# Performance work log

Hardware: AMD Instinct MI355X
Metric: run time of the kernel (lower is better)

## Reference

```python
import jax, jax.numpy as jnp
import numpy as np

B, T, N, FIN, FOUT, EDGE_DIM = 8, 16, 256, 32, 32, 16


def setup_inputs() -> dict:
    key = jax.random.key(0)
    ks = jax.random.split(key, 8)
    def xavier(k, shape):
        fan_in, fan_out = shape[0], shape[1]
        limit = float(np.sqrt(6.0 / (fan_in + fan_out)))
        return jax.random.uniform(k, shape, jnp.float32, -limit, limit)
    return {
        "x": jax.random.normal(ks[0], (B, T, N, FIN), jnp.float32),
        "adj": jax.random.uniform(ks[1], (N, N), jnp.float32),
        # edge_net: Linear(1, edge_dim) -> GELU -> Linear(edge_dim, Fin*Fout)
        "w1": xavier(ks[2], (1, EDGE_DIM)),
        "b1": jnp.zeros((EDGE_DIM,), jnp.float32),
        "w2": xavier(ks[3], (EDGE_DIM, FIN * FOUT)),
        "b2": jnp.zeros((FIN * FOUT,), jnp.float32),
        # node_lin: Linear(Fin, Fout)
        "node_w": xavier(ks[4], (FIN, FOUT)),
        "node_b": jnp.zeros((FOUT,), jnp.float32),
    }


def reference(x, adj, w1, b1, w2, b2, node_w, node_b):
    # edge-conditioned weights: (N, N, Fin, Fout)
    h = jax.nn.gelu(adj[:, :, None] * w1[0] + b1, approximate=False)  # (N,N,E)
    edge_w = (h @ w2 + b2).reshape(N, N, FIN, FOUT)
    # msg[b,t,i,j,:] = sum_f x[b,t,j,f] * edge_w[i,j,f,:]; agg = sum_j msg
    agg = jnp.einsum("btjf,ijfo->btio", x, edge_w)  # (B,T,N,Fout)
    y = jax.nn.gelu(x @ node_w + node_b + agg, approximate=False)
    return y
```

## Files before the change

### kernel.cpp

```cpp
#include <hip/hip_runtime.h>
#include <math.h>

#define NB    256
#define EDIM  16
#define FINN  32
#define FOUTN 32
#define BT    128
#define KKD   4096

typedef __attribute__((ext_vector_type(8))) short short8;
typedef __attribute__((ext_vector_type(4))) float floatx4;

#define MFMA16(a,b,c) __builtin_amdgcn_mfma_f32_16x16x32_bf16((a),(b),(c),0,0,0)

__device__ __forceinline__ float gelu_f(float v) {
    return 0.5f * v * (1.0f + erff(v * 0.70710678118654752f));
}
__device__ __forceinline__ ushort f2bf(float x) {
    union { float f; unsigned u; } v; v.f = x;
    unsigned r = (v.u + 0x7FFFu + ((v.u >> 16) & 1u)) >> 16;
    return (ushort)r;
}
__device__ __forceinline__ float bf2f(ushort b) {
    union { unsigned u; float f; } v; v.u = ((unsigned)b) << 16; return v.f;
}

__global__ __launch_bounds__(256) void h_kernel(const float* __restrict__ adj,
                                                const float* __restrict__ w1,
                                                const float* __restrict__ b1,
                                                const float* __restrict__ w2,
                                                ushort* __restrict__ Hf,
                                                ushort* __restrict__ w2f) {
    int tid = threadIdx.x;
    if (blockIdx.x >= 128) {
        for (int s = 0; s < 2048; s += 256) {
            int slot = s + tid;
            int e = slot >> 7, r = slot & 127;
            int ot = r >> 6, lane = r & 63;
            int m = lane & 15, quad = lane >> 4;
            const float* src = w2 + (size_t)e * 1024 + (quad * 8) * 32 + ot * 16 + m;
            ushort tmp[8];
            #pragma unroll
            for (int i = 0; i < 8; ++i) tmp[i] = f2bf(src[i * 32]);
            *(int4*)(w2f + (size_t)slot * 8) = *(int4*)tmp;
        }
        return;
    }
    __shared__ float adjs[16][264];
    __shared__ float w1s[16], b1s[16];
    int it = blockIdx.x & 15;
    int kq = blockIdx.x >> 4;
    if (tid < 16) { w1s[tid] = w1[tid]; b1s[tid] = b1[tid]; }
    #pragma unroll
    for (int q = 0; q < 4; ++q) {
        int u = q * 256 + tid;
        int row = u >> 6, c4 = u & 63;
        *(float4*)&adjs[row][c4 * 4] =
            ((const float4*)(adj + ((size_t)it * 16 + row) * 256))[c4];
    }
    __syncthreads();
    #pragma unroll
    for (int q = 0; q < 4; ++q) {
        int u = q * 256 + tid;
        int ks = kq * 16 + (u >> 6);
        int lane = u & 63;
        int m = lane & 15, quad = lane >> 4;
        int e = ks >> 3;
        int j0 = (ks & 7) * 32 + quad * 8;
        float w = w1s[e], b = b1s[e];
        ushort tmp[8];
        #pragma unroll
        for (int d = 0; d < 8; ++d)
            tmp[d] = f2bf(gelu_f(adjs[m][j0 + d] * w + b));
        *(int4*)(Hf + (((size_t)it * 128 + ks) * 64 + lane) * 8) = *(int4*)tmp;
    }
}

#define CH   256
#define NCH  16
#define BSP  264
#define XBP  40

__global__ __launch_bounds__(256, 2) void fused_kernel(
        const float* __restrict__ x,      const ushort* __restrict__ w2f,
        const float* __restrict__ b2,     const float* __restrict__ node_w,
        const float* __restrict__ node_b, const ushort* __restrict__ Hf,
        float* __restrict__ out) {
    __shared__ ushort xb[NB][XBP];
    __shared__ ushort Bs[2][32][BSP];
    __shared__ ushort nwT[32][XBP];
    __shared__ float  Sp[8][32];
    __shared__ float  Sv[32];
    __shared__ float  bias2[32];

    int bt   = blockIdx.x;
    int iq   = blockIdx.y;
    int tid  = threadIdx.x;
    int wv   = tid >> 6;
    int lane = tid & 63;
    int m    = lane & 15;
    int quad = lane >> 4;
    int it   = iq * 4 + wv;
    int i0g  = it * 16;

    const ushort* Hlane = Hf + (size_t)it * 128 * 512 + lane * 8;
    const ushort* Wlane = w2f + (size_t)lane * 8;

    short8 areg[2][8];
    short8 wreg[2][2];

    #define ALOAD(dst, c)                                                     \
    {                                                                         \
        _Pragma("unroll")                                                     \
        for (int kk = 0; kk < 8; ++kk)                                        \
            dst[kk] = *(const short8*)(Hlane + ((c) * 8 + kk) * 512);         \
    }
    #define WLOADB(dst, e)                                                    \
    {                                                                         \
        dst[0] = *(const short8*)(Wlane + (size_t)(e) * 1024);                \
        dst[1] = *(const short8*)(Wlane + (size_t)(e) * 1024 + 512);          \
    }

    WLOADB(wreg[0], 0);

    const float4* xg = (const float4*)(x + (size_t)bt * NB * FINN);
    #pragma unroll
    for (int itr = 0; itr < 8; ++itr) {
        int idx4 = itr * 256 + tid;
        float4 v = xg[idx4];
        int j = idx4 >> 3, f = (idx4 & 7) * 4;
        uint2 p;
        p.x = (unsigned)f2bf(v.x) | ((unsigned)f2bf(v.y) << 16);
        p.y = (unsigned)f2bf(v.z) | ((unsigned)f2bf(v.w) << 16);
        *(uint2*)&xb[j][f] = p;
    }
    {
        float4 v = ((const float4*)node_w)[tid];
        int f = tid >> 3, o = (tid & 7) * 4;
        nwT[o + 0][f] = f2bf(v.x); nwT[o + 1][f] = f2bf(v.y);
        nwT[o + 2][f] = f2bf(v.z); nwT[o + 3][f] = f2bf(v.w);
    }
    __syncthreads();

    {
        int f = tid & 31, grp = tid >> 5;
        float s = 0.f;
        for (int j = grp * 32; j < grp * 32 + 32; ++j) s += bf2f(xb[j][f]);
        Sp[grp][f] = s;
    }

    short8 afr[4];
    #pragma unroll
    for (int t = 0; t < 4; ++t)
        afr[t] = *(short8*)&xb[(wv * 4 + t) * 16 + m][quad * 8];

    __syncthreads();
    if (tid < 32) {
        float s = 0.f;
        #pragma unroll
        for (int g = 0; g < 8; ++g) s += Sp[g][tid];
        Sv[tid] = s;
    }

    floatx4 acc[2] = {};

    #define PRODUCE(buf, w)                                                   \
    {                                                                         \
        _Pragma("unroll")                                                     \
        for (int t = 0; t < 4; ++t) {                                         \
            floatx4 z = {0.f, 0.f, 0.f, 0.f};                                 \
            floatx4 d0 = MFMA16(afr[t], w[0], z);                             \
            floatx4 d1 = MFMA16(afr[t], w[1], z);                             \
            int col = (wv * 4 + t) * 16 + quad * 4;                           \
            uint2 p0, p1;                                                     \
            p0.x = (unsigned)f2bf(d0[0]) | ((unsigned)f2bf(d0[1]) << 16);     \
            p0.y = (unsigned)f2bf(d0[2]) | ((unsigned)f2bf(d0[3]) << 16);     \
            p1.x = (unsigned)f2bf(d1[0]) | ((unsigned)f2bf(d1[1]) << 16);     \
            p1.y = (unsigned)f2bf(d1[2]) | ((unsigned)f2bf(d1[3]) << 16);     \
            *(uint2*)&Bs[buf][     m][col] = p0;                              \
            *(uint2*)&Bs[buf][16 + m][col] = p1;                              \
        }                                                                     \
    }
    #define GEMMC(buf, ar)                                                    \
    {                                                                         \
        _Pragma("unroll")                                                     \
        for (int kk = 0; kk < 8; ++kk) {                                      \
            short8 b0 = *(short8*)&Bs[buf][     m][kk * 32 + quad * 8];       \
            short8 b1 = *(short8*)&Bs[buf][16 + m][kk * 32 + quad * 8];       \
            acc[0] = MFMA16(ar[kk], b0, acc[0]);                              \
            acc[1] = MFMA16(ar[kk], b1, acc[1]);                              \
        }                                                                     \
    }

    #pragma unroll
    for (int c = 0; c < NCH; ++c) {
        ALOAD(areg[c & 1], c);
        if (c < NCH - 1) WLOADB(wreg[(c + 1) & 1], c + 1);
        PRODUCE(c & 1, wreg[c & 1]);
        if (c > 0) {
            GEMMC((c - 1) & 1, areg[(c - 1) & 1]);
        } else if (tid < 32) {
            float bb = node_b[tid];
            #pragma unroll
            for (int f = 0; f < FINN; ++f) bb += Sv[f] * b2[f * FOUTN + tid];
            bias2[tid] = bb;
        }
        __syncthreads();
    }
    GEMMC((NCH - 1) & 1, areg[(NCH - 1) & 1]);

    {
        short8 xa = *(short8*)&xb[i0g + m][quad * 8];
        #pragma unroll
        for (int tn = 0; tn < 2; ++tn) {
            short8 nb = *(short8*)&nwT[tn * 16 + m][quad * 8];
            acc[tn] = MFMA16(xa, nb, acc[tn]);
        }
    }
    #pragma unroll
    for (int tn = 0; tn < 2; ++tn) {
        int o = tn * 16 + m;
        float bz = bias2[o];
        #pragma unroll
        for (int r = 0; r < 4; ++r) {
            int row = i0g + quad * 4 + r;
            out[((size_t)bt * NB + row) * FOUTN + o] = gelu_f(acc[tn][r] + bz);
        }
    }
}

extern "C" void kernel_launch(void* const* d_in, const int* in_sizes, int n_in,
                              void* d_out, int out_size, void* d_ws, size_t ws_size,
                              hipStream_t stream) {
    const float* x      = (const float*)d_in[0];
    const float* adj    = (const float*)d_in[1];
    const float* w1     = (const float*)d_in[2];
    const float* b1     = (const float*)d_in[3];
    const float* w2     = (const float*)d_in[4];
    const float* b2     = (const float*)d_in[5];
    const float* node_w = (const float*)d_in[6];
    const float* node_b = (const float*)d_in[7];
    float* out = (float*)d_out;

    ushort* Hf  = (ushort*)d_ws;
    ushort* w2f = Hf + (size_t)NB * KKD;

    hipLaunchKernelGGL(h_kernel, dim3(129), dim3(256), 0, stream,
                       adj, w1, b1, w2, Hf, w2f);
    hipLaunchKernelGGL(fused_kernel, dim3(BT, 4), dim3(256), 0, stream,
                       x, w2f, b2, node_w, node_b, Hf, out);
}
```

Baseline: 96.41 us.

## Give each wave two row tiles and XOR-swizzle the shared B buffer

Each wave now computes two 16-row output tiles instead of one. The grid shrinks from 4 to 2 blocks in y, so the per-(b,t) PRODUCE work that builds the B tile from x and w2 is repeated half as often, and each B fragment read from LDS feeds twice as many MFMAs. The padded Bs row stride is replaced by an XOR swizzle on the column index to avoid LDS bank conflicts without the padding. In exchange, register pressure roughly doubles (16 A fragments per buffer), launch bounds drop to one block per CU, and only 256 blocks are launched.

```diff
diff --git a/kernel.cpp b/kernel.cpp
--- a/kernel.cpp
+++ b/kernel.cpp
@@ -76,44 +76,46 @@
     }
 }
 
-#define CH   256
 #define NCH  16
-#define BSP  264
 #define XBP  40
 
-__global__ __launch_bounds__(256, 2) void fused_kernel(
+__global__ __launch_bounds__(256, 1) void fused_kernel(
         const float* __restrict__ x,      const ushort* __restrict__ w2f,
         const float* __restrict__ b2,     const float* __restrict__ node_w,
         const float* __restrict__ node_b, const ushort* __restrict__ Hf,
         float* __restrict__ out) {
     __shared__ ushort xb[NB][XBP];
-    __shared__ ushort Bs[2][32][BSP];
+    __shared__ ushort Bs[2][32][256];
     __shared__ ushort nwT[32][XBP];
     __shared__ float  Sp[8][32];
     __shared__ float  Sv[32];
     __shared__ float  bias2[32];
 
-    int bt   = blockIdx.x;
-    int iq   = blockIdx.y;
-    int tid  = threadIdx.x;
-    int wv   = tid >> 6;
-    int lane = tid & 63;
-    int m    = lane & 15;
-    int quad = lane >> 4;
-    int it   = iq * 4 + wv;
-    int i0g  = it * 16;
-
-    const ushort* Hlane = Hf + (size_t)it * 128 * 512 + lane * 8;
-    const ushort* Wlane = w2f + (size_t)lane * 8;
-
-    short8 areg[2][8];
+    int bt    = blockIdx.x;
+    int ihalf = blockIdx.y;
+    int tid   = threadIdx.x;
+    int wv    = tid >> 6;
+    int lane  = tid & 63;
+    int m     = lane & 15;
+    int quad  = lane >> 4;
+    int mk    = m & 7;
+    int i0g   = ihalf * 128 + wv * 32;
+    int it0   = i0g >> 4;
+
+    const ushort* Hlane0 = Hf + (size_t)it0 * 128 * 512 + lane * 8;
+    const ushort* Hlane1 = Hlane0 + (size_t)128 * 512;
+    const ushort* Wlane  = w2f + (size_t)lane * 8;
+
+    short8 areg[2][16];
     short8 wreg[2][2];
 
     #define ALOAD(dst, c)                                                     \
     {                                                                         \
         _Pragma("unroll")                                                     \
-        for (int kk = 0; kk < 8; ++kk)                                        \
-            dst[kk] = *(const short8*)(Hlane + ((c) * 8 + kk) * 512);         \
+        for (int kk = 0; kk < 8; ++kk) {                                      \
+            dst[kk]     = *(const short8*)(Hlane0 + ((c) * 8 + kk) * 512);    \
+            dst[8 + kk] = *(const short8*)(Hlane1 + ((c) * 8 + kk) * 512);    \
+        }                                                                     \
     }
     #define WLOADB(dst, e)                                                    \
     {                                                                         \
@@ -162,7 +164,7 @@
         Sv[tid] = s;
     }
 
-    floatx4 acc[2] = {};
+    floatx4 acc[2][2] = {};
 
     #define PRODUCE(buf, w)                                                   \
     {                                                                         \
@@ -171,24 +173,28 @@
             floatx4 z = {0.f, 0.f, 0.f, 0.f};                                 \
             floatx4 d0 = MFMA16(afr[t], w[0], z);                             \
             floatx4 d1 = MFMA16(afr[t], w[1], z);                             \
-            int col = (wv * 4 + t) * 16 + quad * 4;                           \
+            int jt = wv * 4 + t;                                              \
+            int pc = ((((jt * 2 + (quad >> 1)) ^ mk) * 8) + (quad & 1) * 4);  \
             uint2 p0, p1;                                                     \
             p0.x = (unsigned)f2bf(d0[0]) | ((unsigned)f2bf(d0[1]) << 16);     \
             p0.y = (unsigned)f2bf(d0[2]) | ((unsigned)f2bf(d0[3]) << 16);     \
             p1.x = (unsigned)f2bf(d1[0]) | ((unsigned)f2bf(d1[1]) << 16);     \
             p1.y = (unsigned)f2bf(d1[2]) | ((unsigned)f2bf(d1[3]) << 16);     \
-            *(uint2*)&Bs[buf][     m][col] = p0;                              \
-            *(uint2*)&Bs[buf][16 + m][col] = p1;                              \
+            *(uint2*)&Bs[buf][     m][pc] = p0;                               \
+            *(uint2*)&Bs[buf][16 + m][pc] = p1;                               \
         }                                                                     \
     }
     #define GEMMC(buf, ar)                                                    \
     {                                                                         \
         _Pragma("unroll")                                                     \
         for (int kk = 0; kk < 8; ++kk) {                                      \
-            short8 b0 = *(short8*)&Bs[buf][     m][kk * 32 + quad * 8];       \
-            short8 b1 = *(short8*)&Bs[buf][16 + m][kk * 32 + quad * 8];       \
-            acc[0] = MFMA16(ar[kk], b0, acc[0]);                              \
-            acc[1] = MFMA16(ar[kk], b1, acc[1]);                              \
+            int pc = ((kk * 4 + quad) ^ mk) * 8;                              \
+            short8 b0 = *(short8*)&Bs[buf][     m][pc];                       \
+            short8 b1 = *(short8*)&Bs[buf][16 + m][pc];                       \
+            acc[0][0] = MFMA16(ar[kk], b0, acc[0][0]);                        \
+            acc[0][1] = MFMA16(ar[kk], b1, acc[0][1]);                        \
+            acc[1][0] = MFMA16(ar[8 + kk], b0, acc[1][0]);                    \
+            acc[1][1] = MFMA16(ar[8 + kk], b1, acc[1][1]);                    \
         }                                                                     \
     }
 
@@ -209,24 +215,28 @@
     }
     GEMMC((NCH - 1) & 1, areg[(NCH - 1) & 1]);
 
-    {
-        short8 xa = *(short8*)&xb[i0g + m][quad * 8];
+    #pragma unroll
+    for (int tm = 0; tm < 2; ++tm) {
+        short8 xa = *(short8*)&xb[i0g + tm * 16 + m][quad * 8];
         #pragma unroll
         for (int tn = 0; tn < 2; ++tn) {
             short8 nb = *(short8*)&nwT[tn * 16 + m][quad * 8];
-            acc[tn] = MFMA16(xa, nb, acc[tn]);
-        }
-    }
-    #pragma unroll
-    for (int tn = 0; tn < 2; ++tn) {
-        int o = tn * 16 + m;
-        float bz = bias2[o];
-        #pragma unroll
-        for (int r = 0; r < 4; ++r) {
-            int row = i0g + quad * 4 + r;
-            out[((size_t)bt * NB + row) * FOUTN + o] = gelu_f(acc[tn][r] + bz);
-        }
-    }
+            acc[tm][tn] = MFMA16(xa, nb, acc[tm][tn]);
+        }
+    }
+    #pragma unroll
+    for (int tm = 0; tm < 2; ++tm)
+        #pragma unroll
+        for (int tn = 0; tn < 2; ++tn) {
+            int o = tn * 16 + m;
+            float bz = bias2[o];
+            #pragma unroll
+            for (int r = 0; r < 4; ++r) {
+                int row = i0g + tm * 16 + quad * 4 + r;
+                out[((size_t)bt * NB + row) * FOUTN + o] =
+                    gelu_f(acc[tm][tn][r] + bz);
+            }
+        }
 }
 
 extern "C" void kernel_launch(void* const* d_in, const int* in_sizes, int n_in,
@@ -247,6 +257,6 @@
 
     hipLaunchKernelGGL(h_kernel, dim3(129), dim3(256), 0, stream,
                        adj, w1, b1, w2, Hf, w2f);
-    hipLaunchKernelGGL(fused_kernel, dim3(BT, 4), dim3(256), 0, stream,
+    hipLaunchKernelGGL(fused_kernel, dim3(BT, 2), dim3(256), 0, stream,
                        x, w2f, b2, node_w, node_b, Hf, out);
 }
```

Result: slower. 98.53 us (+2.2%).
